# Kernel optimization log

Measured on AMD Instinct MI355X. Metric: run time of the kernel, lower is better.

Reference implementation:

```python
import jax, jax.numpy as jnp
import numpy as np

N = 4096
DIM_IN = 512
DIM_Q = 128
DIM_K = 128
NUM_GRAPHS = 16
NODES_PER_GRAPH = N // NUM_GRAPHS
NEG = -1000000.0


def setup_inputs() -> dict:
    key = jax.random.key(0)
    ks = jax.random.split(key, 10)
    x = jax.random.normal(ks[0], (N, DIM_IN), dtype=jnp.float32)
    b = jax.random.normal(ks[1], (N, N), dtype=jnp.float32)
    c = jax.random.normal(ks[2], (N, N), dtype=jnp.float32)
    sparse_mask = jax.random.randint(ks[3], (N, N), 0, 2).astype(jnp.int32)
    ptr = (jnp.arange(NUM_GRAPHS + 1) * NODES_PER_GRAPH).astype(jnp.int32)
    # linear layer params (q, k, v): y = x @ W.T + bias
    Wq = jax.random.normal(ks[4], (DIM_Q, DIM_IN), dtype=jnp.float32) * 0.02
    bq = jnp.zeros((DIM_Q,), dtype=jnp.float32)
    Wk = jax.random.normal(ks[5], (DIM_K, DIM_IN), dtype=jnp.float32) * 0.02
    bk = jnp.zeros((DIM_K,), dtype=jnp.float32)
    Wv = jax.random.normal(ks[6], (DIM_K, DIM_IN), dtype=jnp.float32) * 0.02
    bv = jnp.zeros((DIM_K,), dtype=jnp.float32)
    return {"x": x, "b": b, "c": c, "ptr": ptr, "sparse_mask": sparse_mask,
            "Wq": Wq, "bq": bq, "Wk": Wk, "bk": bk, "Wv": Wv, "bv": bv}


def reference(x, b, c, ptr, sparse_mask, Wq, bq, Wk, bk, Wv, bv):
    n = x.shape[0]
    q = x @ Wq.T + bq            # [N, dq]
    k = x @ Wk.T + bk            # [N, dk]
    v = x @ Wv.T + bv            # [N, dk]
    # graph id per node from ptr; block-diagonal (same-graph) mask
    gid = jnp.searchsorted(ptr, jnp.arange(n), side='right') - 1
    block = gid[:, None] == gid[None, :]                       # [N, N] bool
    scale = q.shape[-1] ** 0.5
    # compute_a: QK^T/sqrt(dq) on the block diagonal, zeros elsewhere
    a = jnp.where(block, (q @ k.T) / scale, 0.0)
    a = a + b + c
    keep = block & (sparse_mask != 0)
    a = jnp.where(keep, a, NEG)
    sm = jax.nn.softmax(a, axis=-1) * keep.astype(x.dtype)
    return sm @ v
```

## Files before the change

kernel.cpp:

```cpp
#include <hip/hip_runtime.h>
#include <hip/hip_bf16.h>

#define N_NODES 4096
#define DIM_IN 512
#define DIM_QK 128
#define BLK 256
#define NUM_G 16
#define NEGV -1000000.0f

typedef __bf16 bf16x8 __attribute__((ext_vector_type(8)));
typedef float  f32x4  __attribute__((ext_vector_type(4)));

__global__ __launch_bounds__(256) void cvt_kernel(
    const float* __restrict__ x,
    const float* __restrict__ Wq, const float* __restrict__ Wk,
    const float* __restrict__ Wv,
    __bf16* __restrict__ xb, __bf16* __restrict__ wb)
{
    const int i = blockIdx.x * 256 + threadIdx.x;
    if (i < 524288) {
        const float4 v = ((const float4*)x)[i];
        __bf16* o = xb + i * 4;
        o[0] = (__bf16)v.x; o[1] = (__bf16)v.y;
        o[2] = (__bf16)v.z; o[3] = (__bf16)v.w;
    } else {
        const int j = i - 524288;
        if (j < 49152) {
            const int m = j / 16384;
            const float* W = (m == 0) ? Wq : (m == 1 ? Wk : Wv);
            const float4 v = ((const float4*)W)[j - m * 16384];
            __bf16* o = wb + j * 4;
            o[0] = (__bf16)v.x; o[1] = (__bf16)v.y;
            o[2] = (__bf16)v.z; o[3] = (__bf16)v.w;
        }
    }
}

__global__ __launch_bounds__(128) void qkv_mfma(
    const __bf16* __restrict__ xb, const __bf16* __restrict__ wb,
    const float* __restrict__ bq, const float* __restrict__ bk,
    const float* __restrict__ bv,
    __bf16* __restrict__ qb, __bf16* __restrict__ kb, __bf16* __restrict__ vtb)
{
    const int mat    = blockIdx.y >> 1;
    const int colOff = (blockIdx.y & 1) * 64;
    const int wave = threadIdx.x >> 6;
    const int lane = threadIdx.x & 63;
    const int lr   = lane & 15;
    const int quad = lane >> 4;
    const int row0 = blockIdx.x * 32 + wave * 16;

    const __bf16* W    = wb + mat * (DIM_QK * DIM_IN);
    const float*  bias = (mat == 0) ? bq : (mat == 1 ? bk : bv);

    f32x4 acc[4];
    #pragma unroll
    for (int i = 0; i < 4; ++i) acc[i] = (f32x4){0.f, 0.f, 0.f, 0.f};

    const __bf16* arow = xb + (size_t)(row0 + lr) * DIM_IN + quad * 8;
    const __bf16* brow = W + (size_t)(colOff + lr) * DIM_IN + quad * 8;

    #pragma unroll 4
    for (int kt = 0; kt < 16; ++kt) {
        const bf16x8 a = *(const bf16x8*)(arow + kt * 32);
        #pragma unroll
        for (int nt = 0; nt < 4; ++nt) {
            const bf16x8 b = *(const bf16x8*)(brow + nt * 16 * DIM_IN + kt * 32);
            acc[nt] = __builtin_amdgcn_mfma_f32_16x16x32_bf16(a, b, acc[nt], 0, 0, 0);
        }
    }

    #pragma unroll
    for (int nt = 0; nt < 4; ++nt) {
        const int col = colOff + nt * 16 + lr;
        const float bs = bias[col];
        #pragma unroll
        for (int r = 0; r < 4; ++r) {
            const int row = row0 + quad * 4 + r;
            const __bf16 o = (__bf16)(acc[nt][r] + bs);
            if (mat == 0)      qb[(size_t)row * DIM_QK + col] = o;
            else if (mat == 1) kb[(size_t)row * DIM_QK + col] = o;
            else               vtb[(size_t)col * N_NODES + row] = o;
        }
    }
}

#define PSTR 272

__global__ __launch_bounds__(256, 1) void attn_mfma(
    const float* __restrict__ bmat, const float* __restrict__ cmat,
    const int* __restrict__ mask,
    const __bf16* __restrict__ qb, const __bf16* __restrict__ kb,
    const __bf16* __restrict__ vtb,
    float* __restrict__ out)
{
    __shared__ __bf16 plds[16 * PSTR];
    __shared__ float redm[4][16];
    __shared__ float reds[4][16];

    const int tid  = threadIdx.x;
    const int w    = tid >> 6;
    const int lane = tid & 63;
    const int lr   = lane & 15;
    const int quad = lane >> 4;
    const int g    = blockIdx.x >> 4;
    const int tile = blockIdx.x & 15;
    const int row0 = g * BLK + tile * 16;
    const int col0 = g * BLK;

    bf16x8 aq[4];
    #pragma unroll
    for (int kt = 0; kt < 4; ++kt)
        aq[kt] = *(const bf16x8*)(qb + (size_t)(row0 + lr) * DIM_QK + kt * 32 + quad * 8);

    bf16x8 bkf[16];
    #pragma unroll
    for (int kt = 0; kt < 4; ++kt)
        #pragma unroll
        for (int nt = 0; nt < 4; ++nt)
            bkf[kt * 4 + nt] = *(const bf16x8*)(kb
                + (size_t)(col0 + w * 64 + nt * 16 + lr) * DIM_QK + kt * 32 + quad * 8);

    bf16x8 bvf[16];
    #pragma unroll
    for (int nt2 = 0; nt2 < 2; ++nt2)
        #pragma unroll
        for (int kt = 0; kt < 8; ++kt)
            bvf[nt2 * 8 + kt] = *(const bf16x8*)(vtb
                + (size_t)(w * 32 + nt2 * 16 + lr) * N_NODES + col0 + kt * 32 + quad * 8);

    float bbv[16], ccv[16];
    int   mmv[16];
    #pragma unroll
    for (int nt = 0; nt < 4; ++nt)
        #pragma unroll
        for (int r = 0; r < 4; ++r) {
            const size_t idx = (size_t)(row0 + quad * 4 + r) * N_NODES
                             + col0 + w * 64 + nt * 16 + lr;
            bbv[nt * 4 + r] = bmat[idx];
            ccv[nt * 4 + r] = cmat[idx];
            mmv[nt * 4 + r] = mask[idx];
        }

    f32x4 s[4];
    #pragma unroll
    for (int nt = 0; nt < 4; ++nt) s[nt] = (f32x4){0.f, 0.f, 0.f, 0.f};

    #pragma unroll
    for (int kt = 0; kt < 4; ++kt)
        #pragma unroll
        for (int nt = 0; nt < 4; ++nt)
            s[nt] = __builtin_amdgcn_mfma_f32_16x16x32_bf16(aq[kt], bkf[kt * 4 + nt],
                                                            s[nt], 0, 0, 0);

    const float rscale = 0.08838834764831845f;
    #pragma unroll
    for (int nt = 0; nt < 4; ++nt)
        #pragma unroll
        for (int r = 0; r < 4; ++r) {
            const int i = nt * 4 + r;
            s[nt][r] = mmv[i] ? (s[nt][r] * rscale + bbv[i] + ccv[i]) : NEGV;
        }

    float mr[4] = {-3e38f, -3e38f, -3e38f, -3e38f};
    #pragma unroll
    for (int nt = 0; nt < 4; ++nt)
        #pragma unroll
        for (int r = 0; r < 4; ++r) mr[r] = fmaxf(mr[r], s[nt][r]);
    #pragma unroll
    for (int off = 1; off <= 8; off <<= 1)
        #pragma unroll
        for (int r = 0; r < 4; ++r) mr[r] = fmaxf(mr[r], __shfl_xor(mr[r], off));
    if (lr == 0) {
        #pragma unroll
        for (int r = 0; r < 4; ++r) redm[w][quad * 4 + r] = mr[r];
    }
    __syncthreads();
    float M[4];
    #pragma unroll
    for (int r = 0; r < 4; ++r) {
        const int rw = quad * 4 + r;
        M[r] = fmaxf(fmaxf(redm[0][rw], redm[1][rw]), fmaxf(redm[2][rw], redm[3][rw]));
    }

    float sum[4] = {0.f, 0.f, 0.f, 0.f};
    #pragma unroll
    for (int nt = 0; nt < 4; ++nt)
        #pragma unroll
        for (int r = 0; r < 4; ++r) {
            const float e = (s[nt][r] > -1e5f) ? __expf(s[nt][r] - M[r]) : 0.f;
            s[nt][r] = e;
            sum[r] += e;
        }
    #pragma unroll
    for (int off = 1; off <= 8; off <<= 1)
        #pragma unroll
        for (int r = 0; r < 4; ++r) sum[r] += __shfl_xor(sum[r], off);
    if (lr == 0) {
        #pragma unroll
        for (int r = 0; r < 4; ++r) reds[w][quad * 4 + r] = sum[r];
    }
    __syncthreads();
    float inv[4];
    #pragma unroll
    for (int r = 0; r < 4; ++r) {
        const int rw = quad * 4 + r;
        const float t = reds[0][rw] + reds[1][rw] + reds[2][rw] + reds[3][rw];
        inv[r] = (t > 0.f) ? (1.f / t) : 0.f;
    }

    #pragma unroll
    for (int nt = 0; nt < 4; ++nt)
        #pragma unroll
        for (int r = 0; r < 4; ++r)
            plds[(quad * 4 + r) * PSTR + w * 64 + nt * 16 + lr] =
                (__bf16)(s[nt][r] * inv[r]);
    __syncthreads();

    #pragma unroll
    for (int nt2 = 0; nt2 < 2; ++nt2) {
        f32x4 o = (f32x4){0.f, 0.f, 0.f, 0.f};
        #pragma unroll
        for (int kt = 0; kt < 8; ++kt) {
            const bf16x8 a = *(const bf16x8*)(plds + lr * PSTR + kt * 32 + quad * 8);
            o = __builtin_amdgcn_mfma_f32_16x16x32_bf16(a, bvf[nt2 * 8 + kt], o, 0, 0, 0);
        }
        #pragma unroll
        for (int r = 0; r < 4; ++r)
            out[(size_t)(row0 + quad * 4 + r) * DIM_QK + w * 32 + nt2 * 16 + lr] = o[r];
    }
}

extern "C" void kernel_launch(void* const* d_in, const int* in_sizes, int n_in,
                              void* d_out, int out_size, void* d_ws, size_t ws_size,
                              hipStream_t stream) {
    const float* x    = (const float*)d_in[0];
    const float* bmat = (const float*)d_in[1];
    const float* cmat = (const float*)d_in[2];
    const int*   mask = (const int*)d_in[4];
    const float* Wq   = (const float*)d_in[5];
    const float* bq   = (const float*)d_in[6];
    const float* Wk   = (const float*)d_in[7];
    const float* bk   = (const float*)d_in[8];
    const float* Wv   = (const float*)d_in[9];
    const float* bv   = (const float*)d_in[10];
    float* out = (float*)d_out;

    __bf16* xb  = (__bf16*)d_ws;
    __bf16* wb  = xb + (size_t)N_NODES * DIM_IN;
    __bf16* qb  = wb + 3 * DIM_QK * DIM_IN;
    __bf16* kb  = qb + (size_t)N_NODES * DIM_QK;
    __bf16* vtb = kb + (size_t)N_NODES * DIM_QK;

    cvt_kernel<<<dim3((524288 + 49152 + 255) / 256), 256, 0, stream>>>(
        x, Wq, Wk, Wv, xb, wb);

    qkv_mfma<<<dim3(128, 6), 128, 0, stream>>>(
        xb, wb, bq, bk, bv, qb, kb, vtb);

    attn_mfma<<<dim3(NUM_G * 16), 256, 0, stream>>>(
        bmat, cmat, mask, qb, kb, vtb, out);
}
```

Baseline: 196.6 us.

## Fuse convert, QKV projection and attention into one cooperative kernel

Merges the three kernels (fp32-to-bf16 conversion, QKV projection GEMM, and block-diagonal attention) into a single cooperative launch of 256 blocks separated by grid-wide syncs. The QKV stage is remapped so each wave computes a 16-row by 128-column tile (8 MFMA accumulators) over 768 tasks instead of the earlier 64-column split. This targets the launch overhead and inter-kernel gaps. In exchange it adds grid barrier cost, runs the conversion and GEMM stages on only 256 blocks of 256 threads (one block per CU), and raises register pressure in the QKV stage.

```diff
diff --git a/kernel.cpp b/kernel.cpp
--- a/kernel.cpp
+++ b/kernel.cpp
@@ -1,233 +1,242 @@
 #include <hip/hip_runtime.h>
 #include <hip/hip_bf16.h>
+#include <hip/hip_cooperative_groups.h>
+
+namespace cg = cooperative_groups;
 
 #define N_NODES 4096
 #define DIM_IN 512
 #define DIM_QK 128
 #define BLK 256
-#define NUM_G 16
 #define NEGV -1000000.0f
+#define PSTR 272
 
 typedef __bf16 bf16x8 __attribute__((ext_vector_type(8)));
 typedef float  f32x4  __attribute__((ext_vector_type(4)));
 
-__global__ __launch_bounds__(256) void cvt_kernel(
+__global__ __launch_bounds__(256, 1) void fused_attn(
     const float* __restrict__ x,
-    const float* __restrict__ Wq, const float* __restrict__ Wk,
-    const float* __restrict__ Wv,
-    __bf16* __restrict__ xb, __bf16* __restrict__ wb)
-{
-    const int i = blockIdx.x * 256 + threadIdx.x;
-    if (i < 524288) {
-        const float4 v = ((const float4*)x)[i];
-        __bf16* o = xb + i * 4;
-        o[0] = (__bf16)v.x; o[1] = (__bf16)v.y;
-        o[2] = (__bf16)v.z; o[3] = (__bf16)v.w;
-    } else {
-        const int j = i - 524288;
-        if (j < 49152) {
-            const int m = j / 16384;
-            const float* W = (m == 0) ? Wq : (m == 1 ? Wk : Wv);
-            const float4 v = ((const float4*)W)[j - m * 16384];
-            __bf16* o = wb + j * 4;
-            o[0] = (__bf16)v.x; o[1] = (__bf16)v.y;
-            o[2] = (__bf16)v.z; o[3] = (__bf16)v.w;
-        }
-    }
-}
-
-__global__ __launch_bounds__(128) void qkv_mfma(
-    const __bf16* __restrict__ xb, const __bf16* __restrict__ wb,
-    const float* __restrict__ bq, const float* __restrict__ bk,
-    const float* __restrict__ bv,
-    __bf16* __restrict__ qb, __bf16* __restrict__ kb, __bf16* __restrict__ vtb)
-{
-    const int mat    = blockIdx.y >> 1;
-    const int colOff = (blockIdx.y & 1) * 64;
-    const int wave = threadIdx.x >> 6;
-    const int lane = threadIdx.x & 63;
-    const int lr   = lane & 15;
-    const int quad = lane >> 4;
-    const int row0 = blockIdx.x * 32 + wave * 16;
-
-    const __bf16* W    = wb + mat * (DIM_QK * DIM_IN);
-    const float*  bias = (mat == 0) ? bq : (mat == 1 ? bk : bv);
-
-    f32x4 acc[4];
-    #pragma unroll
-    for (int i = 0; i < 4; ++i) acc[i] = (f32x4){0.f, 0.f, 0.f, 0.f};
-
-    const __bf16* arow = xb + (size_t)(row0 + lr) * DIM_IN + quad * 8;
-    const __bf16* brow = W + (size_t)(colOff + lr) * DIM_IN + quad * 8;
-
-    #pragma unroll 4
-    for (int kt = 0; kt < 16; ++kt) {
-        const bf16x8 a = *(const bf16x8*)(arow + kt * 32);
-        #pragma unroll
-        for (int nt = 0; nt < 4; ++nt) {
-            const bf16x8 b = *(const bf16x8*)(brow + nt * 16 * DIM_IN + kt * 32);
-            acc[nt] = __builtin_amdgcn_mfma_f32_16x16x32_bf16(a, b, acc[nt], 0, 0, 0);
-        }
-    }
-
-    #pragma unroll
-    for (int nt = 0; nt < 4; ++nt) {
-        const int col = colOff + nt * 16 + lr;
-        const float bs = bias[col];
-        #pragma unroll
-        for (int r = 0; r < 4; ++r) {
-            const int row = row0 + quad * 4 + r;
-            const __bf16 o = (__bf16)(acc[nt][r] + bs);
-            if (mat == 0)      qb[(size_t)row * DIM_QK + col] = o;
-            else if (mat == 1) kb[(size_t)row * DIM_QK + col] = o;
-            else               vtb[(size_t)col * N_NODES + row] = o;
-        }
-    }
-}
-
-#define PSTR 272
-
-__global__ __launch_bounds__(256, 1) void attn_mfma(
     const float* __restrict__ bmat, const float* __restrict__ cmat,
     const int* __restrict__ mask,
-    const __bf16* __restrict__ qb, const __bf16* __restrict__ kb,
-    const __bf16* __restrict__ vtb,
-    float* __restrict__ out)
+    const float* __restrict__ Wq, const float* __restrict__ bq,
+    const float* __restrict__ Wk, const float* __restrict__ bk,
+    const float* __restrict__ Wv, const float* __restrict__ bv,
+    float* __restrict__ out,
+    __bf16* __restrict__ xb, __bf16* __restrict__ wb,
+    __bf16* __restrict__ qb, __bf16* __restrict__ kb,
+    __bf16* __restrict__ vtb)
 {
     __shared__ __bf16 plds[16 * PSTR];
     __shared__ float redm[4][16];
     __shared__ float reds[4][16];
 
     const int tid  = threadIdx.x;
+    const int bid  = blockIdx.x;
+    const int gtid = bid * 256 + tid;
     const int w    = tid >> 6;
     const int lane = tid & 63;
     const int lr   = lane & 15;
     const int quad = lane >> 4;
-    const int g    = blockIdx.x >> 4;
-    const int tile = blockIdx.x & 15;
-    const int row0 = g * BLK + tile * 16;
-    const int col0 = g * BLK;
-
-    bf16x8 aq[4];
-    #pragma unroll
-    for (int kt = 0; kt < 4; ++kt)
-        aq[kt] = *(const bf16x8*)(qb + (size_t)(row0 + lr) * DIM_QK + kt * 32 + quad * 8);
-
-    bf16x8 bkf[16];
-    #pragma unroll
-    for (int kt = 0; kt < 4; ++kt)
-        #pragma unroll
-        for (int nt = 0; nt < 4; ++nt)
-            bkf[kt * 4 + nt] = *(const bf16x8*)(kb
-                + (size_t)(col0 + w * 64 + nt * 16 + lr) * DIM_QK + kt * 32 + quad * 8);
-
-    bf16x8 bvf[16];
-    #pragma unroll
-    for (int nt2 = 0; nt2 < 2; ++nt2)
-        #pragma unroll
-        for (int kt = 0; kt < 8; ++kt)
-            bvf[nt2 * 8 + kt] = *(const bf16x8*)(vtb
-                + (size_t)(w * 32 + nt2 * 16 + lr) * N_NODES + col0 + kt * 32 + quad * 8);
-
-    float bbv[16], ccv[16];
-    int   mmv[16];
-    #pragma unroll
-    for (int nt = 0; nt < 4; ++nt)
+
+    cg::grid_group grid = cg::this_grid();
+
+    {
+        const float4* xf = (const float4*)x;
+        #pragma unroll
+        for (int i = 0; i < 8; ++i) {
+            const int idx = i * 65536 + gtid;
+            const float4 v = xf[idx];
+            __bf16* o = xb + (size_t)idx * 4;
+            o[0] = (__bf16)v.x; o[1] = (__bf16)v.y;
+            o[2] = (__bf16)v.z; o[3] = (__bf16)v.w;
+        }
+        if (gtid < 49152) {
+            const int m = gtid >> 14;
+            const float* W = (m == 0) ? Wq : (m == 1 ? Wk : Wv);
+            const float4 v = ((const float4*)W)[gtid - (m << 14)];
+            __bf16* o = wb + (size_t)gtid * 4;
+            o[0] = (__bf16)v.x; o[1] = (__bf16)v.y;
+            o[2] = (__bf16)v.z; o[3] = (__bf16)v.w;
+        }
+    }
+
+    __threadfence();
+    grid.sync();
+    __threadfence();
+
+    {
+        const int task = bid * 4 + w;
+        if (task < 768) {
+            const int mat  = task >> 8;
+            const int rt   = task & 255;
+            const int row0 = rt * 16;
+            const __bf16* W    = wb + mat * (DIM_QK * DIM_IN);
+            const float*  bias = (mat == 0) ? bq : (mat == 1 ? bk : bv);
+
+            f32x4 acc[8];
+            #pragma unroll
+            for (int i = 0; i < 8; ++i) acc[i] = (f32x4){0.f, 0.f, 0.f, 0.f};
+
+            const __bf16* arow = xb + (size_t)(row0 + lr) * DIM_IN + quad * 8;
+            const __bf16* brow = W  + (size_t)lr * DIM_IN + quad * 8;
+
+            #pragma unroll 2
+            for (int kt = 0; kt < 16; ++kt) {
+                const bf16x8 a = *(const bf16x8*)(arow + kt * 32);
+                #pragma unroll
+                for (int nt = 0; nt < 8; ++nt) {
+                    const bf16x8 b = *(const bf16x8*)(brow + nt * 16 * DIM_IN + kt * 32);
+                    acc[nt] = __builtin_amdgcn_mfma_f32_16x16x32_bf16(a, b, acc[nt], 0, 0, 0);
+                }
+            }
+
+            #pragma unroll
+            for (int nt = 0; nt < 8; ++nt) {
+                const int col = nt * 16 + lr;
+                const float bs = bias[col];
+                #pragma unroll
+                for (int r = 0; r < 4; ++r) {
+                    const int row = row0 + quad * 4 + r;
+                    const __bf16 o = (__bf16)(acc[nt][r] + bs);
+                    if (mat == 0)      qb[(size_t)row * DIM_QK + col] = o;
+                    else if (mat == 1) kb[(size_t)row * DIM_QK + col] = o;
+                    else               vtb[(size_t)col * N_NODES + row] = o;
+                }
+            }
+        }
+    }
+
+    __threadfence();
+    grid.sync();
+    __threadfence();
+
+    {
+        const int g    = bid >> 4;
+        const int tile = bid & 15;
+        const int row0 = g * BLK + tile * 16;
+        const int col0 = g * BLK;
+
+        bf16x8 aq[4];
+        #pragma unroll
+        for (int kt = 0; kt < 4; ++kt)
+            aq[kt] = *(const bf16x8*)(qb + (size_t)(row0 + lr) * DIM_QK + kt * 32 + quad * 8);
+
+        bf16x8 bkf[16];
+        #pragma unroll
+        for (int kt = 0; kt < 4; ++kt)
+            #pragma unroll
+            for (int nt = 0; nt < 4; ++nt)
+                bkf[kt * 4 + nt] = *(const bf16x8*)(kb
+                    + (size_t)(col0 + w * 64 + nt * 16 + lr) * DIM_QK + kt * 32 + quad * 8);
+
+        bf16x8 bvf[16];
+        #pragma unroll
+        for (int nt2 = 0; nt2 < 2; ++nt2)
+            #pragma unroll
+            for (int kt = 0; kt < 8; ++kt)
+                bvf[nt2 * 8 + kt] = *(const bf16x8*)(vtb
+                    + (size_t)(w * 32 + nt2 * 16 + lr) * N_NODES + col0 + kt * 32 + quad * 8);
+
+        float bbv[16], ccv[16];
+        int   mmv[16];
+        #pragma unroll
+        for (int nt = 0; nt < 4; ++nt)
+            #pragma unroll
+            for (int r = 0; r < 4; ++r) {
+                const size_t idx = (size_t)(row0 + quad * 4 + r) * N_NODES
+                                 + col0 + w * 64 + nt * 16 + lr;
+                bbv[nt * 4 + r] = bmat[idx];
+                ccv[nt * 4 + r] = cmat[idx];
+                mmv[nt * 4 + r] = mask[idx];
+            }
+
+        f32x4 s[4];
+        #pragma unroll
+        for (int nt = 0; nt < 4; ++nt) s[nt] = (f32x4){0.f, 0.f, 0.f, 0.f};
+
+        #pragma unroll
+        for (int kt = 0; kt < 4; ++kt)
+            #pragma unroll
+            for (int nt = 0; nt < 4; ++nt)
+                s[nt] = __builtin_amdgcn_mfma_f32_16x16x32_bf16(aq[kt], bkf[kt * 4 + nt],
+                                                                s[nt], 0, 0, 0);
+
+        const float rscale = 0.08838834764831845f;
+        #pragma unroll
+        for (int nt = 0; nt < 4; ++nt)
+            #pragma unroll
+            for (int r = 0; r < 4; ++r) {
+                const int i = nt * 4 + r;
+                s[nt][r] = mmv[i] ? (s[nt][r] * rscale + bbv[i] + ccv[i]) : NEGV;
+            }
+
+        float mr[4] = {-3e38f, -3e38f, -3e38f, -3e38f};
+        #pragma unroll
+        for (int nt = 0; nt < 4; ++nt)
+            #pragma unroll
+            for (int r = 0; r < 4; ++r) mr[r] = fmaxf(mr[r], s[nt][r]);
+        #pragma unroll
+        for (int off = 1; off <= 8; off <<= 1)
+            #pragma unroll
+            for (int r = 0; r < 4; ++r) mr[r] = fmaxf(mr[r], __shfl_xor(mr[r], off));
+        if (lr == 0) {
+            #pragma unroll
+            for (int r = 0; r < 4; ++r) redm[w][quad * 4 + r] = mr[r];
+        }
+        __syncthreads();
+        float M[4];
         #pragma unroll
         for (int r = 0; r < 4; ++r) {
-            const size_t idx = (size_t)(row0 + quad * 4 + r) * N_NODES
-                             + col0 + w * 64 + nt * 16 + lr;
-            bbv[nt * 4 + r] = bmat[idx];
-            ccv[nt * 4 + r] = cmat[idx];
-            mmv[nt * 4 + r] = mask[idx];
-        }
-
-    f32x4 s[4];
-    #pragma unroll
-    for (int nt = 0; nt < 4; ++nt) s[nt] = (f32x4){0.f, 0.f, 0.f, 0.f};
-
-    #pragma unroll
-    for (int kt = 0; kt < 4; ++kt)
-        #pragma unroll
-        for (int nt = 0; nt < 4; ++nt)
-            s[nt] = __builtin_amdgcn_mfma_f32_16x16x32_bf16(aq[kt], bkf[kt * 4 + nt],
-                                                            s[nt], 0, 0, 0);
-
-    const float rscale = 0.08838834764831845f;
-    #pragma unroll
-    for (int nt = 0; nt < 4; ++nt)
+            const int rw = quad * 4 + r;
+            M[r] = fmaxf(fmaxf(redm[0][rw], redm[1][rw]), fmaxf(redm[2][rw], redm[3][rw]));
+        }
+
+        float sum[4] = {0.f, 0.f, 0.f, 0.f};
+        #pragma unroll
+        for (int nt = 0; nt < 4; ++nt)
+            #pragma unroll
+            for (int r = 0; r < 4; ++r) {
+                const float e = (s[nt][r] > -1e5f) ? __expf(s[nt][r] - M[r]) : 0.f;
+                s[nt][r] = e;
+                sum[r] += e;
+            }
+        #pragma unroll
+        for (int off = 1; off <= 8; off <<= 1)
+            #pragma unroll
+            for (int r = 0; r < 4; ++r) sum[r] += __shfl_xor(sum[r], off);
+        if (lr == 0) {
+            #pragma unroll
+            for (int r = 0; r < 4; ++r) reds[w][quad * 4 + r] = sum[r];
+        }
+        __syncthreads();
+        float inv[4];
         #pragma unroll
         for (int r = 0; r < 4; ++r) {
-            const int i = nt * 4 + r;
-            s[nt][r] = mmv[i] ? (s[nt][r] * rscale + bbv[i] + ccv[i]) : NEGV;
-        }
-
-    float mr[4] = {-3e38f, -3e38f, -3e38f, -3e38f};
-    #pragma unroll
-    for (int nt = 0; nt < 4; ++nt)
-        #pragma unroll
-        for (int r = 0; r < 4; ++r) mr[r] = fmaxf(mr[r], s[nt][r]);
-    #pragma unroll
-    for (int off = 1; off <= 8; off <<= 1)
-        #pragma unroll
-        for (int r = 0; r < 4; ++r) mr[r] = fmaxf(mr[r], __shfl_xor(mr[r], off));
-    if (lr == 0) {
-        #pragma unroll
-        for (int r = 0; r < 4; ++r) redm[w][quad * 4 + r] = mr[r];
-    }
-    __syncthreads();
-    float M[4];
-    #pragma unroll
-    for (int r = 0; r < 4; ++r) {
-        const int rw = quad * 4 + r;
-        M[r] = fmaxf(fmaxf(redm[0][rw], redm[1][rw]), fmaxf(redm[2][rw], redm[3][rw]));
-    }
-
-    float sum[4] = {0.f, 0.f, 0.f, 0.f};
-    #pragma unroll
-    for (int nt = 0; nt < 4; ++nt)
-        #pragma unroll
-        for (int r = 0; r < 4; ++r) {
-            const float e = (s[nt][r] > -1e5f) ? __expf(s[nt][r] - M[r]) : 0.f;
-            s[nt][r] = e;
-            sum[r] += e;
-        }
-    #pragma unroll
-    for (int off = 1; off <= 8; off <<= 1)
-        #pragma unroll
-        for (int r = 0; r < 4; ++r) sum[r] += __shfl_xor(sum[r], off);
-    if (lr == 0) {
-        #pragma unroll
-        for (int r = 0; r < 4; ++r) reds[w][quad * 4 + r] = sum[r];
-    }
-    __syncthreads();
-    float inv[4];
-    #pragma unroll
-    for (int r = 0; r < 4; ++r) {
-        const int rw = quad * 4 + r;
-        const float t = reds[0][rw] + reds[1][rw] + reds[2][rw] + reds[3][rw];
-        inv[r] = (t > 0.f) ? (1.f / t) : 0.f;
-    }
-
-    #pragma unroll
-    for (int nt = 0; nt < 4; ++nt)
-        #pragma unroll
-        for (int r = 0; r < 4; ++r)
-            plds[(quad * 4 + r) * PSTR + w * 64 + nt * 16 + lr] =
-                (__bf16)(s[nt][r] * inv[r]);
-    __syncthreads();
-
-    #pragma unroll
-    for (int nt2 = 0; nt2 < 2; ++nt2) {
-        f32x4 o = (f32x4){0.f, 0.f, 0.f, 0.f};
-        #pragma unroll
-        for (int kt = 0; kt < 8; ++kt) {
-            const bf16x8 a = *(const bf16x8*)(plds + lr * PSTR + kt * 32 + quad * 8);
-            o = __builtin_amdgcn_mfma_f32_16x16x32_bf16(a, bvf[nt2 * 8 + kt], o, 0, 0, 0);
-        }
-        #pragma unroll
-        for (int r = 0; r < 4; ++r)
-            out[(size_t)(row0 + quad * 4 + r) * DIM_QK + w * 32 + nt2 * 16 + lr] = o[r];
+            const int rw = quad * 4 + r;
+            const float t = reds[0][rw] + reds[1][rw] + reds[2][rw] + reds[3][rw];
+            inv[r] = (t > 0.f) ? (1.f / t) : 0.f;
+        }
+
+        #pragma unroll
+        for (int nt = 0; nt < 4; ++nt)
+            #pragma unroll
+            for (int r = 0; r < 4; ++r)
+                plds[(quad * 4 + r) * PSTR + w * 64 + nt * 16 + lr] =
+                    (__bf16)(s[nt][r] * inv[r]);
+        __syncthreads();
+
+        #pragma unroll
+        for (int nt2 = 0; nt2 < 2; ++nt2) {
+            f32x4 o = (f32x4){0.f, 0.f, 0.f, 0.f};
+            #pragma unroll
+            for (int kt = 0; kt < 8; ++kt) {
+                const bf16x8 a = *(const bf16x8*)(plds + lr * PSTR + kt * 32 + quad * 8);
+                o = __builtin_amdgcn_mfma_f32_16x16x32_bf16(a, bvf[nt2 * 8 + kt], o, 0, 0, 0);
+            }
+            #pragma unroll
+            for (int r = 0; r < 4; ++r)
+                out[(size_t)(row0 + quad * 4 + r) * DIM_QK + w * 32 + nt2 * 16 + lr] = o[r];
+        }
     }
 }
 
@@ -252,12 +261,11 @@
     __bf16* kb  = qb + (size_t)N_NODES * DIM_QK;
     __bf16* vtb = kb + (size_t)N_NODES * DIM_QK;
 
-    cvt_kernel<<<dim3((524288 + 49152 + 255) / 256), 256, 0, stream>>>(
-        x, Wq, Wk, Wv, xb, wb);
-
-    qkv_mfma<<<dim3(128, 6), 128, 0, stream>>>(
-        xb, wb, bq, bk, bv, qb, kb, vtb);
-
-    attn_mfma<<<dim3(NUM_G * 16), 256, 0, stream>>>(
-        bmat, cmat, mask, qb, kb, vtb, out);
+    void* args[] = {
+        (void*)&x, (void*)&bmat, (void*)&cmat, (void*)&mask,
+        (void*)&Wq, (void*)&bq, (void*)&Wk, (void*)&bk, (void*)&Wv, (void*)&bv,
+        (void*)&out, (void*)&xb, (void*)&wb, (void*)&qb, (void*)&kb, (void*)&vtb
+    };
+    hipLaunchCooperativeKernel((void*)fused_attn, dim3(256), dim3(256),
+                               args, 0, stream);
 }
```

New measurement: 348.7 us. 1.77x slower.
